# Kernel tuning notes

Hardware: AMD Instinct MI355X
Metric: run time of the kernel (lower is better)

Reference implementation:

```python
import jax, jax.numpy as jnp
import numpy as np

B, D, H, NG = 8192, 2048, 2048, 7  # batch, input_size, hidden_size, num gate networks


def setup_inputs() -> dict:
    key = jax.random.key(0)
    ks = jax.random.split(key, 7)
    hx = jax.random.normal(ks[0], (B, D), dtype=jnp.float32)
    cx1 = jax.random.normal(ks[1], (B, H), dtype=jnp.float32)
    cx2 = jax.random.normal(ks[2], (B, H), dtype=jnp.float32)
    tj = jax.random.uniform(ks[3], (B, 1), dtype=jnp.float32)
    dt = jax.random.uniform(ks[4], (B, 1), dtype=jnp.float32)
    # fused weights for the 7 gate/decay networks, order: i1,i2,f1,f2,o,z,d
    W = jax.random.normal(ks[5], (D, NG * H), dtype=jnp.float32) * (1.0 / np.sqrt(D))
    b = jax.random.normal(ks[6], (NG * H,), dtype=jnp.float32) * 0.01
    return {"hx": hx, "cx1": cx1, "cx2": cx2, "tj": tj, "dt": dt, "W": W, "b": b}


def reference(hx, cx1, cx2, tj, dt, W, b):
    # One fused GEMM for all 7 gate networks, then split.
    g = hx @ W + b  # [B, 7H]
    i1, i2, f1, f2, o, z_raw, d_raw = [g[:, k * H:(k + 1) * H] for k in range(NG)]
    sig = jax.nn.sigmoid
    i1, i2, f1, f2, o = sig(i1), sig(i2), sig(f1), sig(f2), sig(o)
    z = jnp.tanh(z_raw)                 # Tanh(LC_z(hx)) as in forward
    decay = jax.nn.softplus(d_raw)      # Decay_network: positive decay coeff
    cy1 = f1 * cx1 + i1 * z             # fast cell state
    cy2 = f2 * cx2 + i2 * z             # asymptotic cell state
    t = tj + dt
    # continuous-time decay: c(t) = cy2 + (cy1 - cy2) * exp(-decay * (t - tj))
    c_t = cy2 + (cy1 - cy2) * jnp.exp(-decay * (t - tj))
    h_t = o * jnp.tanh(c_t)             # get_h(t)
    return jnp.stack([cy1, cy2, h_t])   # [3, B, H]
```

## Files before the change

### kernel.cpp

```cpp
#include <hip/hip_runtime.h>
#include <hip/hip_bf16.h>
#include <stdint.h>


#define B_SZ 8192
#define D_SZ 2048
#define H_SZ 2048
#define NG   7
#define NW   (NG * H_SZ)
#define BM   256
#define BN   32
#define BK   32
#define NKST (D_SZ / BK)
#define NBX  (B_SZ / BM)
#define NBY  (H_SZ / BN)

#define WB_BYTES   ((size_t)NBY * NKST * 14336)
#define HXB_OFF    WB_BYTES
#define HXB_BYTES  ((size_t)NBX * NKST * 16384)
#define WS_NEEDED  (WB_BYTES + HXB_BYTES)

typedef __attribute__((ext_vector_type(8))) short bf16x8;
typedef __attribute__((ext_vector_type(4))) float f32x4;

__device__ __forceinline__ uint32_t cvtpk(float lo, float hi) {
    uint32_t r;
    asm("v_cvt_pk_bf16_f32 %0, %1, %2" : "=v"(r) : "v"(lo), "v"(hi));
    return r;
}
__device__ __forceinline__ void glds16(const void* g, void* l) {
    __builtin_amdgcn_global_load_lds(
        (const __attribute__((address_space(1))) uint32_t*)g,
        (__attribute__((address_space(3))) uint32_t*)l, 16, 0, 0);
}
__device__ __forceinline__ float sigmoidf_(float x) {
    return 1.0f / (1.0f + __expf(-x));
}
__device__ __forceinline__ float tanhf_(float x) {
    float ax = fabsf(x);
    float e = __expf(2.0f * ax);
    float t = 1.0f - 2.0f / (e + 1.0f);
    return copysignf(t, x);
}
__device__ __forceinline__ float softplusf_(float x) {
    return (x > 30.0f) ? x : __logf(1.0f + __expf(x));
}

__global__ __launch_bounds__(896) void conv_w(const float* __restrict__ W,
                                              char* __restrict__ wb)
{
    const int by = blockIdx.x >> 6;
    const int ks = blockIdx.x & 63;
    const int u  = threadIdx.x;
    const int r  = u >> 2;
    const int pc = u & 3;
    const int koct = pc ^ ((r >> 1) & 3);
    const int g  = r >> 5;
    const int n  = r & 31;
    const int col = g * H_SZ + by * BN + n;
    const float* src = W + (size_t)(ks * BK + koct * 8) * NW + col;
    float w0 = src[0];
    float w1 = src[(size_t)NW];
    float w2 = src[(size_t)2 * NW];
    float w3 = src[(size_t)3 * NW];
    float w4 = src[(size_t)4 * NW];
    float w5 = src[(size_t)5 * NW];
    float w6 = src[(size_t)6 * NW];
    float w7 = src[(size_t)7 * NW];
    uint4 o;
    o.x = cvtpk(w0, w1); o.y = cvtpk(w2, w3);
    o.z = cvtpk(w4, w5); o.w = cvtpk(w6, w7);
    *(uint4*)(wb + (size_t)blockIdx.x * 14336 + u * 16) = o;
}

__global__ __launch_bounds__(1024) void conv_hx(const float* __restrict__ hx,
                                                char* __restrict__ hxb)
{
    const int bx = blockIdx.x >> 6;
    const int ks = blockIdx.x & 63;
    const int u  = threadIdx.x;
    const int r  = u >> 2;
    const int pc = u & 3;
    const int koct = pc ^ ((r >> 1) & 3);
    const float* src = hx + (size_t)(bx * BM + r) * D_SZ + ks * BK + koct * 8;
    f32x4 a = *(const f32x4*)(src);
    f32x4 b = *(const f32x4*)(src + 4);
    uint4 o;
    o.x = cvtpk(a[0], a[1]); o.y = cvtpk(a[2], a[3]);
    o.z = cvtpk(b[0], b[1]); o.w = cvtpk(b[2], b[3]);
    *(uint4*)(hxb + (size_t)blockIdx.x * 16384 + u * 16) = o;
}

#define NTH3 1024
#define BUFB 30720
#define NBUF 4

#define PIPE_WAIT(N)                                        \
    asm volatile("s_waitcnt vmcnt(" #N ")" ::: "memory");   \
    __builtin_amdgcn_s_barrier();                           \
    asm volatile("" ::: "memory");

__global__ __launch_bounds__(NTH3, 4) void lstm_bf16(
    const char* __restrict__ wb, const char* __restrict__ hxb,
    const float* __restrict__ cx1, const float* __restrict__ cx2,
    const float* __restrict__ dt, const float* __restrict__ bias,
    float* __restrict__ out)
{
    __shared__ char smem[NBUF * BUFB];

    const int tid  = threadIdx.x;
    const int lane = tid & 63;
    const int wid  = tid >> 6;
    const int wm   = wid >> 1;
    const int wn   = wid & 1;
    const int l15  = lane & 15;
    const int lg   = lane >> 4;

    const int b0  = blockIdx.x;
    const int swz = (b0 & 7) * 256 + (b0 >> 3);
    const int by2 = swz >> 6;
    const int rem = swz & 63;
    const int bx  = rem >> 1;
    const int by  = by2 * 2 + (rem & 1);
    const int gm0 = bx * BM;
    const int n0  = by * BN;

    const size_t hx_tile0 = (size_t)(bx * NKST) << 14;
    const size_t w_tile0  = (size_t)(by * NKST) * 14336;

    const int xch  = (lg ^ ((l15 >> 1) & 3)) * 8;
    const int aoff0 = (wm * 32 + l15) * 32 + xch;
    const int aoff1 = aoff0 + 16 * 32;
    int boff[NG];
    #pragma unroll
    for (int g = 0; g < NG; ++g)
        boff[g] = (g * 32 + wn * 16 + l15) * 32 + xch;

    f32x4 acc[NG][2];
    #pragma unroll
    for (int g = 0; g < NG; ++g) {
        acc[g][0] = (f32x4){0.f, 0.f, 0.f, 0.f};
        acc[g][1] = (f32x4){0.f, 0.f, 0.f, 0.f};
    }

    const int lane16 = lane << 4;

    auto stage = [&](int c, int k) {
        {
            const char* src = hxb + hx_tile0 + ((size_t)k << 14) + (wid << 10) + lane16;
            glds16(src, smem + c * BUFB + (wid << 10));
        }
        if (lane < 56) {
            const char* src = wb + w_tile0 + (size_t)k * 14336 + wid * 896 + lane16;
            glds16(src, smem + c * BUFB + 16384 + wid * 896);
        }
    };

    auto compute = [&](int c) {
        const ushort* sa = (const ushort*)(smem + c * BUFB);
        const ushort* sb = (const ushort*)(smem + c * BUFB + 16384);
        bf16x8 af0 = *(const bf16x8*)(sa + aoff0);
        bf16x8 af1 = *(const bf16x8*)(sa + aoff1);
        #pragma unroll
        for (int g = 0; g < NG; ++g) {
            bf16x8 bfr = *(const bf16x8*)(sb + boff[g]);
            acc[g][0] = __builtin_amdgcn_mfma_f32_16x16x32_bf16(af0, bfr, acc[g][0], 0, 0, 0);
            acc[g][1] = __builtin_amdgcn_mfma_f32_16x16x32_bf16(af1, bfr, acc[g][1], 0, 0, 0);
        }
    };

    stage(0, 0);
    stage(1, 1);
    stage(2, 2);

    for (int t = 0; t < NKST - 3; ++t) {
        PIPE_WAIT(4)
        stage((t + 3) & 3, t + 3);
        compute(t & 3);
    }
    PIPE_WAIT(4)
    compute((NKST - 3) & 3);
    PIPE_WAIT(2)
    compute((NKST - 2) & 3);
    PIPE_WAIT(0)
    compute((NKST - 1) & 3);

    const size_t BH = (size_t)B_SZ * H_SZ;
    const int j = n0 + wn * 16 + l15;
    float bj[NG];
    #pragma unroll
    for (int g = 0; g < NG; ++g) bj[g] = bias[g * H_SZ + j];

    #pragma unroll
    for (int mf = 0; mf < 2; ++mf) {
        #pragma unroll
        for (int r = 0; r < 4; ++r) {
            int row = gm0 + wm * 32 + mf * 16 + lg * 4 + r;
            float dtv = dt[row];
            float i1 = sigmoidf_(acc[0][mf][r] + bj[0]);
            float i2 = sigmoidf_(acc[1][mf][r] + bj[1]);
            float f1 = sigmoidf_(acc[2][mf][r] + bj[2]);
            float f2 = sigmoidf_(acc[3][mf][r] + bj[3]);
            float o  = sigmoidf_(acc[4][mf][r] + bj[4]);
            float z  = tanhf_(acc[5][mf][r] + bj[5]);
            float dec = softplusf_(acc[6][mf][r] + bj[6]);
            size_t idx = (size_t)row * H_SZ + j;
            float c1 = cx1[idx], c2 = cx2[idx];
            float cy1 = f1 * c1 + i1 * z;
            float cy2 = f2 * c2 + i2 * z;
            float ct  = cy2 + (cy1 - cy2) * __expf(-dec * dtv);
            float ht  = o * tanhf_(ct);
            out[idx]          = cy1;
            out[BH + idx]     = cy2;
            out[2 * BH + idx] = ht;
        }
    }
}

#define NTH  512
#define LDP  40
__global__ __launch_bounds__(NTH, 2) void lstm_f32(
    const float* __restrict__ hx, const float* __restrict__ cx1,
    const float* __restrict__ cx2, const float* __restrict__ dt,
    const float* __restrict__ W, const float* __restrict__ bias,
    float* __restrict__ out)
{
    __shared__ ushort sA[BM * LDP];
    __shared__ ushort sB[NG * BN * LDP];

    const int tid = threadIdx.x;
    const int nwg = gridDim.x;
    const int cpx = nwg >> 3;
    const int b0  = blockIdx.x;
    const int swz = (b0 & 7) * cpx + (b0 >> 3);
    const int bx  = swz & 31;
    const int by  = swz >> 5;
    const int gm0 = bx * BM;
    const int n0  = by * BN;

    const int lane = tid & 63;
    const int wid  = tid >> 6;
    const int wm   = wid >> 1;
    const int wn   = wid & 1;
    const int l15  = lane & 15;
    const int lg   = lane >> 4;

    const int ar0 = tid >> 2,          aq0 = tid & 3;
    const int ar1 = (tid + 512) >> 2,  aq1 = tid & 3;
    const bool hasB = (tid < 448);
    const int bg  = tid >> 6;
    const int bkq = (tid >> 3) & 7;
    const int bnq = tid & 7;

    f32x4 pa[4];
    f32x4 pb[4];

    auto issue_loads = [&](int K0) {
        {
            const float* p = hx + (size_t)(gm0 + ar0) * D_SZ + K0 + aq0 * 8;
            pa[0] = *(const f32x4*)(p);
            pa[1] = *(const f32x4*)(p + 4);
        }
        {
            const float* p = hx + (size_t)(gm0 + ar1) * D_SZ + K0 + aq1 * 8;
            pa[2] = *(const f32x4*)(p);
            pa[3] = *(const f32x4*)(p + 4);
        }
        if (hasB) {
            const float* p = W + (size_t)(K0 + bkq * 4) * NW + bg * H_SZ + n0 + bnq * 4;
            pb[0] = *(const f32x4*)(p);
            pb[1] = *(const f32x4*)(p + NW);
            pb[2] = *(const f32x4*)(p + 2 * NW);
            pb[3] = *(const f32x4*)(p + 3 * NW);
        }
    };

    auto store_lds = [&]() {
        {
            uint4 u;
            u.x = cvtpk(pa[0][0], pa[0][1]); u.y = cvtpk(pa[0][2], pa[0][3]);
            u.z = cvtpk(pa[1][0], pa[1][1]); u.w = cvtpk(pa[1][2], pa[1][3]);
            *(uint4*)(&sA[ar0 * LDP + aq0 * 8]) = u;
        }
        {
            uint4 u;
            u.x = cvtpk(pa[2][0], pa[2][1]); u.y = cvtpk(pa[2][2], pa[2][3]);
            u.z = cvtpk(pa[3][0], pa[3][1]); u.w = cvtpk(pa[3][2], pa[3][3]);
            *(uint4*)(&sA[ar1 * LDP + aq1 * 8]) = u;
        }
        if (hasB) {
            #pragma unroll
            for (int jj = 0; jj < 4; ++jj) {
                uint2 v;
                v.x = cvtpk(pb[0][jj], pb[1][jj]);
                v.y = cvtpk(pb[2][jj], pb[3][jj]);
                *(uint2*)(&sB[(bg * BN + bnq * 4 + jj) * LDP + bkq * 4]) = v;
            }
        }
    };

    f32x4 acc[NG][4];
    #pragma unroll
    for (int g = 0; g < NG; ++g)
        #pragma unroll
        for (int mf = 0; mf < 4; ++mf)
            acc[g][mf] = (f32x4){0.f, 0.f, 0.f, 0.f};

    int aoff[4];
    #pragma unroll
    for (int mf = 0; mf < 4; ++mf)
        aoff[mf] = (wm * 64 + mf * 16 + l15) * LDP + lg * 8;
    int boff[NG];
    #pragma unroll
    for (int g = 0; g < NG; ++g)
        boff[g] = (g * BN + wn * 16 + l15) * LDP + lg * 8;

    issue_loads(0);
    for (int kk = 0; kk < NKST; ++kk) {
        store_lds();
        __syncthreads();
        if (kk + 1 < NKST) issue_loads((kk + 1) * BK);

        bf16x8 af[4];
        #pragma unroll
        for (int mf = 0; mf < 4; ++mf)
            af[mf] = *(const bf16x8*)(&sA[aoff[mf]]);
        #pragma unroll
        for (int g = 0; g < NG; ++g) {
            bf16x8 bfr = *(const bf16x8*)(&sB[boff[g]]);
            #pragma unroll
            for (int mf = 0; mf < 4; ++mf)
                acc[g][mf] = __builtin_amdgcn_mfma_f32_16x16x32_bf16(
                    af[mf], bfr, acc[g][mf], 0, 0, 0);
        }
        __syncthreads();
    }

    const size_t BH = (size_t)B_SZ * H_SZ;
    const int j = n0 + wn * 16 + l15;
    float bj[NG];
    #pragma unroll
    for (int g = 0; g < NG; ++g) bj[g] = bias[g * H_SZ + j];

    #pragma unroll
    for (int mf = 0; mf < 4; ++mf) {
        #pragma unroll
        for (int r = 0; r < 4; ++r) {
            int row = gm0 + wm * 64 + mf * 16 + lg * 4 + r;
            float dtv = dt[row];
            float i1 = sigmoidf_(acc[0][mf][r] + bj[0]);
            float i2 = sigmoidf_(acc[1][mf][r] + bj[1]);
            float f1 = sigmoidf_(acc[2][mf][r] + bj[2]);
            float f2 = sigmoidf_(acc[3][mf][r] + bj[3]);
            float o  = sigmoidf_(acc[4][mf][r] + bj[4]);
            float z  = tanhf_(acc[5][mf][r] + bj[5]);
            float dec = softplusf_(acc[6][mf][r] + bj[6]);
            size_t idx = (size_t)row * H_SZ + j;
            float c1 = cx1[idx], c2 = cx2[idx];
            float cy1 = f1 * c1 + i1 * z;
            float cy2 = f2 * c2 + i2 * z;
            float ct  = cy2 + (cy1 - cy2) * __expf(-dec * dtv);
            float ht  = o * tanhf_(ct);
            out[idx]          = cy1;
            out[BH + idx]     = cy2;
            out[2 * BH + idx] = ht;
        }
    }
}

extern "C" void kernel_launch(void* const* d_in, const int* in_sizes, int n_in,
                              void* d_out, int out_size, void* d_ws, size_t ws_size,
                              hipStream_t stream) {
    const float* hx  = (const float*)d_in[0];
    const float* cx1 = (const float*)d_in[1];
    const float* cx2 = (const float*)d_in[2];
    const float* dt  = (const float*)d_in[4];
    const float* W   = (const float*)d_in[5];
    const float* b   = (const float*)d_in[6];
    float* out = (float*)d_out;

    if (ws_size >= WS_NEEDED) {
        char* wb  = (char*)d_ws;
        char* hxb = (char*)d_ws + HXB_OFF;
        conv_w<<<dim3(NBY * NKST), dim3(896), 0, stream>>>(W, wb);
        conv_hx<<<dim3(NBX * NKST), dim3(1024), 0, stream>>>(hx, hxb);
        lstm_bf16<<<dim3(NBX * NBY), dim3(NTH3), 0, stream>>>(
            wb, hxb, cx1, cx2, dt, b, out);
    } else {
        lstm_f32<<<dim3(NBX * NBY), dim3(NTH), 0, stream>>>(
            hx, cx1, cx2, dt, W, b, out);
    }
}
```

Baseline: 543.9 us.

## Halve bf16 GEMM block threads and give each wave four M fragments

Cuts the bf16 LSTM kernel from 16 to 8 waves per block. Each wave now covers 64 rows (four 16-row MFMA fragments) instead of 32, so every B fragment read from LDS feeds four MFMAs. Staging now issues two global-to-LDS copies per thread, the vmcnt waits are doubled to match, and the MFMA section is wrapped in s_setprio. The aim is fewer LDS reads per MFMA, at the cost of fewer waves to hide latency and more accumulator registers per thread.

```diff
diff --git a/kernel.cpp b/kernel.cpp
--- a/kernel.cpp
+++ b/kernel.cpp
@@ -91,7 +91,7 @@
     *(uint4*)(hxb + (size_t)blockIdx.x * 16384 + u * 16) = o;
 }
 
-#define NTH3 1024
+#define NTH3 512
 #define BUFB 30720
 #define NBUF 4
 
@@ -100,7 +100,7 @@
     __builtin_amdgcn_s_barrier();                           \
     asm volatile("" ::: "memory");
 
-__global__ __launch_bounds__(NTH3, 4) void lstm_bf16(
+__global__ __launch_bounds__(NTH3, 2) void lstm_bf16(
     const char* __restrict__ wb, const char* __restrict__ hxb,
     const float* __restrict__ cx1, const float* __restrict__ cx2,
     const float* __restrict__ dt, const float* __restrict__ bias,
@@ -129,212 +129,73 @@
     const size_t w_tile0  = (size_t)(by * NKST) * 14336;
 
     const int xch  = (lg ^ ((l15 >> 1) & 3)) * 8;
-    const int aoff0 = (wm * 32 + l15) * 32 + xch;
-    const int aoff1 = aoff0 + 16 * 32;
+    int aoff[4];
+    #pragma unroll
+    for (int mf = 0; mf < 4; ++mf)
+        aoff[mf] = (wm * 64 + mf * 16 + l15) * 32 + xch;
     int boff[NG];
     #pragma unroll
     for (int g = 0; g < NG; ++g)
         boff[g] = (g * 32 + wn * 16 + l15) * 32 + xch;
 
-    f32x4 acc[NG][2];
-    #pragma unroll
-    for (int g = 0; g < NG; ++g) {
-        acc[g][0] = (f32x4){0.f, 0.f, 0.f, 0.f};
-        acc[g][1] = (f32x4){0.f, 0.f, 0.f, 0.f};
-    }
+    f32x4 acc[NG][4];
+    #pragma unroll
+    for (int g = 0; g < NG; ++g)
+        #pragma unroll
+        for (int mf = 0; mf < 4; ++mf)
+            acc[g][mf] = (f32x4){0.f, 0.f, 0.f, 0.f};
 
     const int lane16 = lane << 4;
 
     auto stage = [&](int c, int k) {
         {
-            const char* src = hxb + hx_tile0 + ((size_t)k << 14) + (wid << 10) + lane16;
-            glds16(src, smem + c * BUFB + (wid << 10));
-        }
-        if (lane < 56) {
-            const char* src = wb + w_tile0 + (size_t)k * 14336 + wid * 896 + lane16;
-            glds16(src, smem + c * BUFB + 16384 + wid * 896);
+            const char* src = hxb + hx_tile0 + ((size_t)k << 14) + (wid << 11) + lane16;
+            char* dst = smem + c * BUFB + (wid << 11);
+            glds16(src, dst);
+            glds16(src + 1024, dst + 1024);
+        }
+        {
+            const char* src = wb + w_tile0 + (size_t)k * 14336 + wid * 1792 + lane16;
+            char* dst = smem + c * BUFB + 16384 + wid * 1792;
+            glds16(src, dst);
+            if (lane < 48) glds16(src + 1024, dst + 1024);
         }
     };
 
     auto compute = [&](int c) {
         const ushort* sa = (const ushort*)(smem + c * BUFB);
         const ushort* sb = (const ushort*)(smem + c * BUFB + 16384);
-        bf16x8 af0 = *(const bf16x8*)(sa + aoff0);
-        bf16x8 af1 = *(const bf16x8*)(sa + aoff1);
+        bf16x8 af[4];
+        #pragma unroll
+        for (int mf = 0; mf < 4; ++mf)
+            af[mf] = *(const bf16x8*)(sa + aoff[mf]);
+        __builtin_amdgcn_s_setprio(1);
         #pragma unroll
         for (int g = 0; g < NG; ++g) {
             bf16x8 bfr = *(const bf16x8*)(sb + boff[g]);
-            acc[g][0] = __builtin_amdgcn_mfma_f32_16x16x32_bf16(af0, bfr, acc[g][0], 0, 0, 0);
-            acc[g][1] = __builtin_amdgcn_mfma_f32_16x16x32_bf16(af1, bfr, acc[g][1], 0, 0, 0);
-        }
-    };
-
-    stage(0, 0);
-    stage(1, 1);
-    stage(2, 2);
-
-    for (int t = 0; t < NKST - 3; ++t) {
-        PIPE_WAIT(4)
-        stage((t + 3) & 3, t + 3);
-        compute(t & 3);
-    }
-    PIPE_WAIT(4)
-    compute((NKST - 3) & 3);
-    PIPE_WAIT(2)
-    compute((NKST - 2) & 3);
-    PIPE_WAIT(0)
-    compute((NKST - 1) & 3);
-
-    const size_t BH = (size_t)B_SZ * H_SZ;
-    const int j = n0 + wn * 16 + l15;
-    float bj[NG];
-    #pragma unroll
-    for (int g = 0; g < NG; ++g) bj[g] = bias[g * H_SZ + j];
-
-    #pragma unroll
-    for (int mf = 0; mf < 2; ++mf) {
-        #pragma unroll
-        for (int r = 0; r < 4; ++r) {
-            int row = gm0 + wm * 32 + mf * 16 + lg * 4 + r;
-            float dtv = dt[row];
-            float i1 = sigmoidf_(acc[0][mf][r] + bj[0]);
-            float i2 = sigmoidf_(acc[1][mf][r] + bj[1]);
-            float f1 = sigmoidf_(acc[2][mf][r] + bj[2]);
-            float f2 = sigmoidf_(acc[3][mf][r] + bj[3]);
-            float o  = sigmoidf_(acc[4][mf][r] + bj[4]);
-            float z  = tanhf_(acc[5][mf][r] + bj[5]);
-            float dec = softplusf_(acc[6][mf][r] + bj[6]);
-            size_t idx = (size_t)row * H_SZ + j;
-            float c1 = cx1[idx], c2 = cx2[idx];
-            float cy1 = f1 * c1 + i1 * z;
-            float cy2 = f2 * c2 + i2 * z;
-            float ct  = cy2 + (cy1 - cy2) * __expf(-dec * dtv);
-            float ht  = o * tanhf_(ct);
-            out[idx]          = cy1;
-            out[BH + idx]     = cy2;
-            out[2 * BH + idx] = ht;
-        }
-    }
-}
-
-#define NTH  512
-#define LDP  40
-__global__ __launch_bounds__(NTH, 2) void lstm_f32(
-    const float* __restrict__ hx, const float* __restrict__ cx1,
-    const float* __restrict__ cx2, const float* __restrict__ dt,
-    const float* __restrict__ W, const float* __restrict__ bias,
-    float* __restrict__ out)
-{
-    __shared__ ushort sA[BM * LDP];
-    __shared__ ushort sB[NG * BN * LDP];
-
-    const int tid = threadIdx.x;
-    const int nwg = gridDim.x;
-    const int cpx = nwg >> 3;
-    const int b0  = blockIdx.x;
-    const int swz = (b0 & 7) * cpx + (b0 >> 3);
-    const int bx  = swz & 31;
-    const int by  = swz >> 5;
-    const int gm0 = bx * BM;
-    const int n0  = by * BN;
-
-    const int lane = tid & 63;
-    const int wid  = tid >> 6;
-    const int wm   = wid >> 1;
-    const int wn   = wid & 1;
-    const int l15  = lane & 15;
-    const int lg   = lane >> 4;
-
-    const int ar0 = tid >> 2,          aq0 = tid & 3;
-    const int ar1 = (tid + 512) >> 2,  aq1 = tid & 3;
-    const bool hasB = (tid < 448);
-    const int bg  = tid >> 6;
-    const int bkq = (tid >> 3) & 7;
-    const int bnq = tid & 7;
-
-    f32x4 pa[4];
-    f32x4 pb[4];
-
-    auto issue_loads = [&](int K0) {
-        {
-            const float* p = hx + (size_t)(gm0 + ar0) * D_SZ + K0 + aq0 * 8;
-            pa[0] = *(const f32x4*)(p);
-            pa[1] = *(const f32x4*)(p + 4);
-        }
-        {
-            const float* p = hx + (size_t)(gm0 + ar1) * D_SZ + K0 + aq1 * 8;
-            pa[2] = *(const f32x4*)(p);
-            pa[3] = *(const f32x4*)(p + 4);
-        }
-        if (hasB) {
-            const float* p = W + (size_t)(K0 + bkq * 4) * NW + bg * H_SZ + n0 + bnq * 4;
-            pb[0] = *(const f32x4*)(p);
-            pb[1] = *(const f32x4*)(p + NW);
-            pb[2] = *(const f32x4*)(p + 2 * NW);
-            pb[3] = *(const f32x4*)(p + 3 * NW);
-        }
-    };
-
-    auto store_lds = [&]() {
-        {
-            uint4 u;
-            u.x = cvtpk(pa[0][0], pa[0][1]); u.y = cvtpk(pa[0][2], pa[0][3]);
-            u.z = cvtpk(pa[1][0], pa[1][1]); u.w = cvtpk(pa[1][2], pa[1][3]);
-            *(uint4*)(&sA[ar0 * LDP + aq0 * 8]) = u;
-        }
-        {
-            uint4 u;
-            u.x = cvtpk(pa[2][0], pa[2][1]); u.y = cvtpk(pa[2][2], pa[2][3]);
-            u.z = cvtpk(pa[3][0], pa[3][1]); u.w = cvtpk(pa[3][2], pa[3][3]);
-            *(uint4*)(&sA[ar1 * LDP + aq1 * 8]) = u;
-        }
-        if (hasB) {
-            #pragma unroll
-            for (int jj = 0; jj < 4; ++jj) {
-                uint2 v;
-                v.x = cvtpk(pb[0][jj], pb[1][jj]);
-                v.y = cvtpk(pb[2][jj], pb[3][jj]);
-                *(uint2*)(&sB[(bg * BN + bnq * 4 + jj) * LDP + bkq * 4]) = v;
-            }
-        }
-    };
-
-    f32x4 acc[NG][4];
-    #pragma unroll
-    for (int g = 0; g < NG; ++g)
-        #pragma unroll
-        for (int mf = 0; mf < 4; ++mf)
-            acc[g][mf] = (f32x4){0.f, 0.f, 0.f, 0.f};
-
-    int aoff[4];
-    #pragma unroll
-    for (int mf = 0; mf < 4; ++mf)
-        aoff[mf] = (wm * 64 + mf * 16 + l15) * LDP + lg * 8;
-    int boff[NG];
-    #pragma unroll
-    for (int g = 0; g < NG; ++g)
-        boff[g] = (g * BN + wn * 16 + l15) * LDP + lg * 8;
-
-    issue_loads(0);
-    for (int kk = 0; kk < NKST; ++kk) {
-        store_lds();
-        __syncthreads();
-        if (kk + 1 < NKST) issue_loads((kk + 1) * BK);
-
-        bf16x8 af[4];
-        #pragma unroll
-        for (int mf = 0; mf < 4; ++mf)
-            af[mf] = *(const bf16x8*)(&sA[aoff[mf]]);
-        #pragma unroll
-        for (int g = 0; g < NG; ++g) {
-            bf16x8 bfr = *(const bf16x8*)(&sB[boff[g]]);
             #pragma unroll
             for (int mf = 0; mf < 4; ++mf)
                 acc[g][mf] = __builtin_amdgcn_mfma_f32_16x16x32_bf16(
                     af[mf], bfr, acc[g][mf], 0, 0, 0);
         }
-        __syncthreads();
+        __builtin_amdgcn_s_setprio(0);
+    };
+
+    stage(0, 0);
+    stage(1, 1);
+    stage(2, 2);
+
+    for (int t = 0; t < NKST - 3; ++t) {
+        PIPE_WAIT(8)
+        stage((t + 3) & 3, t + 3);
+        compute(t & 3);
     }
+    PIPE_WAIT(8)
+    compute((NKST - 3) & 3);
+    PIPE_WAIT(4)
+    compute((NKST - 2) & 3);
+    PIPE_WAIT(0)
+    compute((NKST - 1) & 3);
 
     const size_t BH = (size_t)B_SZ * H_SZ;
     const int j = n0 + wn * 16 + l15;
@@ -368,6 +229,157 @@
     }
 }
 
+#define NTH  512
+#define LDP  40
+__global__ __launch_bounds__(NTH, 2) void lstm_f32(
+    const float* __restrict__ hx, const float* __restrict__ cx1,
+    const float* __restrict__ cx2, const float* __restrict__ dt,
+    const float* __restrict__ W, const float* __restrict__ bias,
+    float* __restrict__ out)
+{
+    __shared__ ushort sA[BM * LDP];
+    __shared__ ushort sB[NG * BN * LDP];
+
+    const int tid = threadIdx.x;
+    const int nwg = gridDim.x;
+    const int cpx = nwg >> 3;
+    const int b0  = blockIdx.x;
+    const int swz = (b0 & 7) * cpx + (b0 >> 3);
+    const int bx  = swz & 31;
+    const int by  = swz >> 5;
+    const int gm0 = bx * BM;
+    const int n0  = by * BN;
+
+    const int lane = tid & 63;
+    const int wid  = tid >> 6;
+    const int wm   = wid >> 1;
+    const int wn   = wid & 1;
+    const int l15  = lane & 15;
+    const int lg   = lane >> 4;
+
+    const int ar0 = tid >> 2,          aq0 = tid & 3;
+    const int ar1 = (tid + 512) >> 2,  aq1 = tid & 3;
+    const bool hasB = (tid < 448);
+    const int bg  = tid >> 6;
+    const int bkq = (tid >> 3) & 7;
+    const int bnq = tid & 7;
+
+    f32x4 pa[4];
+    f32x4 pb[4];
+
+    auto issue_loads = [&](int K0) {
+        {
+            const float* p = hx + (size_t)(gm0 + ar0) * D_SZ + K0 + aq0 * 8;
+            pa[0] = *(const f32x4*)(p);
+            pa[1] = *(const f32x4*)(p + 4);
+        }
+        {
+            const float* p = hx + (size_t)(gm0 + ar1) * D_SZ + K0 + aq1 * 8;
+            pa[2] = *(const f32x4*)(p);
+            pa[3] = *(const f32x4*)(p + 4);
+        }
+        if (hasB) {
+            const float* p = W + (size_t)(K0 + bkq * 4) * NW + bg * H_SZ + n0 + bnq * 4;
+            pb[0] = *(const f32x4*)(p);
+            pb[1] = *(const f32x4*)(p + NW);
+            pb[2] = *(const f32x4*)(p + 2 * NW);
+            pb[3] = *(const f32x4*)(p + 3 * NW);
+        }
+    };
+
+    auto store_lds = [&]() {
+        {
+            uint4 u;
+            u.x = cvtpk(pa[0][0], pa[0][1]); u.y = cvtpk(pa[0][2], pa[0][3]);
+            u.z = cvtpk(pa[1][0], pa[1][1]); u.w = cvtpk(pa[1][2], pa[1][3]);
+            *(uint4*)(&sA[ar0 * LDP + aq0 * 8]) = u;
+        }
+        {
+            uint4 u;
+            u.x = cvtpk(pa[2][0], pa[2][1]); u.y = cvtpk(pa[2][2], pa[2][3]);
+            u.z = cvtpk(pa[3][0], pa[3][1]); u.w = cvtpk(pa[3][2], pa[3][3]);
+            *(uint4*)(&sA[ar1 * LDP + aq1 * 8]) = u;
+        }
+        if (hasB) {
+            #pragma unroll
+            for (int jj = 0; jj < 4; ++jj) {
+                uint2 v;
+                v.x = cvtpk(pb[0][jj], pb[1][jj]);
+                v.y = cvtpk(pb[2][jj], pb[3][jj]);
+                *(uint2*)(&sB[(bg * BN + bnq * 4 + jj) * LDP + bkq * 4]) = v;
+            }
+        }
+    };
+
+    f32x4 acc[NG][4];
+    #pragma unroll
+    for (int g = 0; g < NG; ++g)
+        #pragma unroll
+        for (int mf = 0; mf < 4; ++mf)
+            acc[g][mf] = (f32x4){0.f, 0.f, 0.f, 0.f};
+
+    int aoff[4];
+    #pragma unroll
+    for (int mf = 0; mf < 4; ++mf)
+        aoff[mf] = (wm * 64 + mf * 16 + l15) * LDP + lg * 8;
+    int boff[NG];
+    #pragma unroll
+    for (int g = 0; g < NG; ++g)
+        boff[g] = (g * BN + wn * 16 + l15) * LDP + lg * 8;
+
+    issue_loads(0);
+    for (int kk = 0; kk < NKST; ++kk) {
+        store_lds();
+        __syncthreads();
+        if (kk + 1 < NKST) issue_loads((kk + 1) * BK);
+
+        bf16x8 af[4];
+        #pragma unroll
+        for (int mf = 0; mf < 4; ++mf)
+            af[mf] = *(const bf16x8*)(&sA[aoff[mf]]);
+        #pragma unroll
+        for (int g = 0; g < NG; ++g) {
+            bf16x8 bfr = *(const bf16x8*)(&sB[boff[g]]);
+            #pragma unroll
+            for (int mf = 0; mf < 4; ++mf)
+                acc[g][mf] = __builtin_amdgcn_mfma_f32_16x16x32_bf16(
+                    af[mf], bfr, acc[g][mf], 0, 0, 0);
+        }
+        __syncthreads();
+    }
+
+    const size_t BH = (size_t)B_SZ * H_SZ;
+    const int j = n0 + wn * 16 + l15;
+    float bj[NG];
+    #pragma unroll
+    for (int g = 0; g < NG; ++g) bj[g] = bias[g * H_SZ + j];
+
+    #pragma unroll
+    for (int mf = 0; mf < 4; ++mf) {
+        #pragma unroll
+        for (int r = 0; r < 4; ++r) {
+            int row = gm0 + wm * 64 + mf * 16 + lg * 4 + r;
+            float dtv = dt[row];
+            float i1 = sigmoidf_(acc[0][mf][r] + bj[0]);
+            float i2 = sigmoidf_(acc[1][mf][r] + bj[1]);
+            float f1 = sigmoidf_(acc[2][mf][r] + bj[2]);
+            float f2 = sigmoidf_(acc[3][mf][r] + bj[3]);
+            float o  = sigmoidf_(acc[4][mf][r] + bj[4]);
+            float z  = tanhf_(acc[5][mf][r] + bj[5]);
+            float dec = softplusf_(acc[6][mf][r] + bj[6]);
+            size_t idx = (size_t)row * H_SZ + j;
+            float c1 = cx1[idx], c2 = cx2[idx];
+            float cy1 = f1 * c1 + i1 * z;
+            float cy2 = f2 * c2 + i2 * z;
+            float ct  = cy2 + (cy1 - cy2) * __expf(-dec * dtv);
+            float ht  = o * tanhf_(ct);
+            out[idx]          = cy1;
+            out[BH + idx]     = cy2;
+            out[2 * BH + idx] = ht;
+        }
+    }
+}
+
 extern "C" void kernel_launch(void* const* d_in, const int* in_sizes, int n_in,
                               void* d_out, int out_size, void* d_ws, size_t ws_size,
                               hipStream_t stream) {
```

Result: no change. 553.6 us (+1.8%).
